# Kernel tuning notes

Hardware: AMD Instinct MI355X
Metric: run time of the kernel (lower is better)

Reference implementation:

```python
import jax, jax.numpy as jnp
import numpy as np

D_MODEL = 1024
N_HEADS = 16
RANK = 128
N_COMPRESS = 16
N_KNOWLEDGE = 32768
KNOWLEDGE_K = 8
B, S = 4, 1024
EPS = 1e-5


def setup_inputs() -> dict:
    key = jax.random.key(0)
    ks = jax.random.split(key, 16)
    inp = {
        'x': jax.random.normal(ks[0], (B, S, D_MODEL), jnp.float32),
        'mask': jnp.tril(jnp.ones((S, S), bool))[None, None],  # causal [1,1,S,S]
        'compress_neurons': jax.random.normal(ks[1], (N_COMPRESS, D_MODEL, RANK), jnp.float32) / np.sqrt(D_MODEL),
        'knowledge_K': jax.random.normal(ks[2], (N_KNOWLEDGE, RANK), jnp.float32) * 0.02,
        'knowledge_V': jax.random.normal(ks[3], (N_KNOWLEDGE, D_MODEL), jnp.float32) * 0.02,
        'router_Q': jax.random.normal(ks[4], (D_MODEL, N_COMPRESS), jnp.float32) * 0.02,
        'router_K': jax.random.normal(ks[5], (D_MODEL, N_COMPRESS), jnp.float32) * 0.02,
        'router_V': jax.random.normal(ks[6], (D_MODEL, N_COMPRESS), jnp.float32) * 0.02,
        'router_M': jax.random.normal(ks[7], (D_MODEL, N_COMPRESS), jnp.float32) * 0.02,
        'W_Q': jax.random.normal(ks[8], (RANK, D_MODEL), jnp.float32) / np.sqrt(RANK),
        'W_K': jax.random.normal(ks[9], (RANK, D_MODEL), jnp.float32) / np.sqrt(RANK),
        'W_V': jax.random.normal(ks[10], (RANK, D_MODEL), jnp.float32) / np.sqrt(RANK),
        'W_O': jax.random.normal(ks[11], (D_MODEL, D_MODEL), jnp.float32) / np.sqrt(D_MODEL),
        'ln1_g': jnp.ones((D_MODEL,), jnp.float32),
        'ln1_b': jnp.zeros((D_MODEL,), jnp.float32),
        'ln2_g': jnp.ones((D_MODEL,), jnp.float32),
        'ln2_b': jnp.zeros((D_MODEL,), jnp.float32),
    }
    return inp


def _layernorm(x, g, b):
    mu = x.mean(-1, keepdims=True)
    var = ((x - mu) ** 2).mean(-1, keepdims=True)
    return (x - mu) * jax.lax.rsqrt(var + EPS) * g + b


def _compress(x, router_W, neurons):
    # x: [B,S,D]; router_W: [D,N]; neurons: [N,D,R]
    weights = jax.nn.softmax(x @ router_W, axis=-1)               # [B,S,N]
    all_proj = jnp.einsum('bsd,ndr->bsnr', x, neurons)            # [B,S,N,R]
    return jnp.einsum('bsnr,bsn->bsr', all_proj, weights)         # [B,S,R]


def reference(x, mask, compress_neurons, knowledge_K, knowledge_V,
              router_Q, router_K, router_V, router_M,
              W_Q, W_K, W_V, W_O, ln1_g, ln1_b, ln2_g, ln2_b):
    d_head = D_MODEL // N_HEADS
    h = _layernorm(x, ln1_g, ln1_b)
    # soft-routed low-rank compression for Q/K/V
    hQ = _compress(h, router_Q, compress_neurons)
    hK = _compress(h, router_K, compress_neurons)
    hV = _compress(h, router_V, compress_neurons)
    Q = (hQ @ W_Q).reshape(B, S, N_HEADS, d_head).transpose(0, 2, 1, 3)
    K = (hK @ W_K).reshape(B, S, N_HEADS, d_head).transpose(0, 2, 1, 3)
    V = (hV @ W_V).reshape(B, S, N_HEADS, d_head).transpose(0, 2, 1, 3)
    scores = jnp.einsum('bhqd,bhkd->bhqk', Q, K) / np.sqrt(d_head)
    scores = jnp.where(mask, scores, -jnp.inf)
    attn = jax.nn.softmax(scores, axis=-1)
    attn_out = jnp.einsum('bhqk,bhkd->bhqd', attn, V)
    attn_out = attn_out.transpose(0, 2, 1, 3).reshape(B, S, D_MODEL)
    x = x + attn_out @ W_O
    # knowledge memory
    h2 = _layernorm(x, ln2_g, ln2_b)
    Qm = _compress(h2, router_M, compress_neurons)                # [B,S,R]
    kscores = Qm @ knowledge_K.T / np.sqrt(RANK)                  # [B,S,NK]
    topk_scores, topk_idx = jax.lax.top_k(kscores, KNOWLEDGE_K)
    kweights = jax.nn.softmax(topk_scores, axis=-1)               # [B,S,k]
    selected_V = knowledge_V[topk_idx]                            # [B,S,k,D]
    mem_out = jnp.einsum('bskd,bsk->bsd', selected_V, kweights)
    return x + mem_out
```

## Files before the change

### kernel.cpp

```cpp
#include <hip/hip_runtime.h>
#include <math.h>

#define DM     1024
#define RANK   128
#define NCMP   16
#define NKNOW  32768
#define TOPK   8
#define NROWS  4096
#define NEG_BIG -3.0e38f
#define TK_SPLIT 32
#define TK_KEYS (NKNOW / TK_SPLIT)

typedef __attribute__((ext_vector_type(8))) short s8v;
typedef __attribute__((ext_vector_type(4))) float f4v;

__device__ __forceinline__ unsigned short f2bf(float f) {
  union { float fl; unsigned u; } v; v.fl = f;
  return (unsigned short)((v.u + 0x7FFFu + ((v.u >> 16) & 1u)) >> 16);
}
__device__ __forceinline__ float bf2f(unsigned short u) {
  return __uint_as_float((unsigned)u << 16);
}
__device__ __forceinline__ f4v mfma16(s8v a, s8v b, f4v c) {
  return __builtin_amdgcn_mfma_f32_16x16x32_bf16(a, b, c, 0, 0, 0);
}
__device__ __forceinline__ unsigned umed3(unsigned a, unsigned b, unsigned c) {
  unsigned d;
  asm("v_med3_u32 %0, %1, %2, %3" : "=v"(d) : "v"(a), "v"(b), "v"(c));
  return d;
}
__device__ __forceinline__ void gload16(const unsigned short* g, unsigned short* l) {
  __builtin_amdgcn_global_load_lds(
      (const __attribute__((address_space(1))) unsigned int*)(g),
      (__attribute__((address_space(3))) unsigned int*)(l), 16, 0, 0);
}

__global__ __launch_bounds__(256) void ln_kernel(const float* __restrict__ x,
                                                 const float* __restrict__ g,
                                                 const float* __restrict__ b,
                                                 unsigned short* __restrict__ obf) {
  __shared__ float red1[4], red2[4];
  const int row = blockIdx.x, t = threadIdx.x;
  const float4 v = reinterpret_cast<const float4*>(x + (size_t)row * DM)[t];
  float s = v.x + v.y + v.z + v.w;
#pragma unroll
  for (int m = 1; m <= 32; m <<= 1) s += __shfl_xor(s, m);
  if ((t & 63) == 0) red1[t >> 6] = s;
  __syncthreads();
  const float mu = (red1[0] + red1[1] + red1[2] + red1[3]) * (1.0f / DM);
  const float dx = v.x - mu, dy = v.y - mu, dz = v.z - mu, dw = v.w - mu;
  float ss = dx * dx + dy * dy + dz * dz + dw * dw;
#pragma unroll
  for (int m = 1; m <= 32; m <<= 1) ss += __shfl_xor(ss, m);
  if ((t & 63) == 0) red2[t >> 6] = ss;
  __syncthreads();
  const float var = (red2[0] + red2[1] + red2[2] + red2[3]) * (1.0f / DM);
  const float inv = rsqrtf(var + 1e-5f);
  const float4 g4 = reinterpret_cast<const float4*>(g)[t];
  const float4 b4 = reinterpret_cast<const float4*>(b)[t];
  ushort4 u = make_ushort4(f2bf(dx * inv * g4.x + b4.x), f2bf(dy * inv * g4.y + b4.y),
                           f2bf(dz * inv * g4.z + b4.z), f2bf(dw * inv * g4.w + b4.w));
  reinterpret_cast<ushort4*>(obf + (size_t)row * DM)[t] = u;
}

__global__ __launch_bounds__(256) void tcvt_kernel(const float* __restrict__ in,
                                                   unsigned short* __restrict__ out,
                                                   int K, int N) {
  __shared__ float ld[32][33];
  const int bb = blockIdx.z;
  const int k0 = blockIdx.y * 32, n0 = blockIdx.x * 32;
  const int t = threadIdx.x;
  const float* ib = in + (size_t)bb * K * N;
  unsigned short* ob = out + (size_t)bb * K * N;
  const int kl = t >> 3, nl = (t & 7) * 4;
  const float4 v = *reinterpret_cast<const float4*>(&ib[(size_t)(k0 + kl) * N + n0 + nl]);
  ld[kl][nl] = v.x; ld[kl][nl + 1] = v.y; ld[kl][nl + 2] = v.z; ld[kl][nl + 3] = v.w;
  __syncthreads();
  const int nw = t >> 3, kw = (t & 7) * 4;
  ushort4 o = make_ushort4(f2bf(ld[kw][nw]), f2bf(ld[kw + 1][nw]),
                           f2bf(ld[kw + 2][nw]), f2bf(ld[kw + 3][nw]));
  *reinterpret_cast<ushort4*>(&ob[(size_t)(n0 + nw) * K + k0 + kw]) = o;
}

__global__ __launch_bounds__(256) void vtr_kernel(const unsigned short* __restrict__ V,
                                                  unsigned short* __restrict__ Vt) {
  __shared__ unsigned short ld[32][40];
  const int bh = blockIdx.z, b = bh >> 4, hh = bh & 15;
  const int s0 = blockIdx.x * 32, d0 = blockIdx.y * 32;
  const int t = threadIdx.x;
  const int r = t >> 3, c = (t & 7) * 4;
  *reinterpret_cast<ushort4*>(&ld[r][c]) =
      *reinterpret_cast<const ushort4*>(&V[(size_t)(b * 1024 + s0 + r) * DM + hh * 64 + d0 + c]);
  __syncthreads();
  ushort4 o;
  o.x = ld[c + 0][r]; o.y = ld[c + 1][r]; o.z = ld[c + 2][r]; o.w = ld[c + 3][r];
  *reinterpret_cast<ushort4*>(&Vt[((size_t)bh * 64 + d0 + r) * 1024 + s0 + c]) = o;
}

__global__ __launch_bounds__(256) void cvt_kernel(const float* __restrict__ in,
                                                  unsigned short* __restrict__ out, int n8) {
  const int i = blockIdx.x * 256 + threadIdx.x;
  if (i < n8) {
    const float4 a = reinterpret_cast<const float4*>(in)[2 * i];
    const float4 b = reinterpret_cast<const float4*>(in)[2 * i + 1];
    reinterpret_cast<ushort4*>(out)[2 * i] =
        make_ushort4(f2bf(a.x), f2bf(a.y), f2bf(a.z), f2bf(a.w));
    reinterpret_cast<ushort4*>(out)[2 * i + 1] =
        make_ushort4(f2bf(b.x), f2bf(b.y), f2bf(b.z), f2bf(b.w));
  }
}

__global__ __launch_bounds__(256) void router3_kernel(const unsigned short* __restrict__ h,
                                                      const float* __restrict__ R0,
                                                      const float* __restrict__ R1,
                                                      const float* __restrict__ R2,
                                                      float* __restrict__ w0,
                                                      float* __restrict__ w1,
                                                      float* __restrict__ w2) {
  __shared__ float hs[DM];
  __shared__ float red[3][16][17];
  const int row = blockIdx.x, t = threadIdx.x;
  {
    const ushort4 u = reinterpret_cast<const ushort4*>(h + (size_t)row * DM)[t];
    hs[t * 4 + 0] = bf2f(u.x); hs[t * 4 + 1] = bf2f(u.y);
    hs[t * 4 + 2] = bf2f(u.z); hs[t * 4 + 3] = bf2f(u.w);
  }
  __syncthreads();
  const int o = t & 15, seg = t >> 4;
  float a0 = 0.f, a1 = 0.f, a2 = 0.f;
  for (int d = seg * 64; d < seg * 64 + 64; ++d) {
    const float hv = hs[d];
    a0 += hv * R0[d * NCMP + o];
    a1 += hv * R1[d * NCMP + o];
    a2 += hv * R2[d * NCMP + o];
  }
  red[0][seg][o] = a0; red[1][seg][o] = a1; red[2][seg][o] = a2;
  __syncthreads();
  if (t < 48) {
    const int g = t >> 4, oo = t & 15;
    float dot = 0.f;
#pragma unroll
    for (int s = 0; s < 16; ++s) dot += red[g][s][oo];
    float m = dot;
#pragma unroll
    for (int msk = 1; msk < 16; msk <<= 1) m = fmaxf(m, __shfl_xor(m, msk));
    const float e = __expf(dot - m);
    float ssum = e;
#pragma unroll
    for (int msk = 1; msk < 16; msk <<= 1) ssum += __shfl_xor(ssum, msk);
    float* wp = (g == 0) ? w0 : (g == 1) ? w1 : w2;
    wp[(size_t)row * NCMP + oo] = e / ssum;
  }
}

__global__ __launch_bounds__(256) void router_kernel(const unsigned short* __restrict__ h,
                                                     const float* __restrict__ R,
                                                     float* __restrict__ w) {
  __shared__ float hs[DM];
  __shared__ float red[16][17];
  const int row = blockIdx.x, t = threadIdx.x;
  {
    const ushort4 u = reinterpret_cast<const ushort4*>(h + (size_t)row * DM)[t];
    hs[t * 4 + 0] = bf2f(u.x); hs[t * 4 + 1] = bf2f(u.y);
    hs[t * 4 + 2] = bf2f(u.z); hs[t * 4 + 3] = bf2f(u.w);
  }
  __syncthreads();
  const int o = t & 15, seg = t >> 4;
  float acc = 0.f;
  for (int d = seg * 64; d < seg * 64 + 64; ++d) acc += hs[d] * R[d * NCMP + o];
  red[seg][o] = acc;
  __syncthreads();
  if (t < 16) {
    float dot = 0.f;
#pragma unroll
    for (int s = 0; s < 16; ++s) dot += red[s][t];
    float m = dot;
#pragma unroll
    for (int msk = 1; msk < 16; msk <<= 1) m = fmaxf(m, __shfl_xor(m, msk));
    const float e = __expf(dot - m);
    float ssum = e;
#pragma unroll
    for (int msk = 1; msk < 16; msk <<= 1) ssum += __shfl_xor(ssum, msk);
    w[(size_t)row * NCMP + t] = e / ssum;
  }
}

template <bool OUT_BF16, bool RES>
__global__ __launch_bounds__(256) void mfma_nt(const unsigned short* __restrict__ A,
                                               const unsigned short* __restrict__ B,
                                               float* __restrict__ Cf,
                                               unsigned short* __restrict__ Cb,
                                               const float* __restrict__ res,
                                               int M, int N, int K, int bshift) {
  __shared__ unsigned short As[128 * 64];
  __shared__ unsigned short Bs[128 * 64];
  const int t = threadIdx.x;
  const int lane = t & 63, w = t >> 6;
  const int wm = w >> 1, wn = w & 1;
  const int bm = blockIdx.y, bn = blockIdx.x;
  const int l15 = lane & 15, l4 = lane >> 4;
  f4v acc[4][4] = {};
  const int srow = w * 32 + (lane >> 3);
  const int scol = ((lane & 7) ^ (lane >> 3)) * 8;
  const unsigned short* ga = A + (size_t)(bm * 128 + srow) * K + scol;
  const unsigned short* gb = B + (size_t)(bm >> bshift) * ((size_t)N * K) +
                             (size_t)(bn * 128 + srow) * K + scol;
  unsigned short* const lA = &As[w * 2048];
  unsigned short* const lB = &Bs[w * 2048];
  for (int k0 = 0; k0 < K; k0 += 64) {
#pragma unroll
    for (int j = 0; j < 4; ++j) {
      gload16(ga + (size_t)j * 8 * K + k0, lA + j * 512);
      gload16(gb + (size_t)j * 8 * K + k0, lB + j * 512);
    }
    __syncthreads();
#pragma unroll
    for (int ks = 0; ks < 2; ++ks) {
      s8v af[4], bf[4];
      const int sc = (ks * 32 + l4 * 8) ^ ((l15 & 7) * 8);
#pragma unroll
      for (int i = 0; i < 4; ++i) {
        af[i] = *reinterpret_cast<const s8v*>(&As[(wm * 64 + i * 16 + l15) * 64 + sc]);
        bf[i] = *reinterpret_cast<const s8v*>(&Bs[(wn * 64 + i * 16 + l15) * 64 + sc]);
      }
#pragma unroll
      for (int i = 0; i < 4; ++i)
#pragma unroll
        for (int j = 0; j < 4; ++j) acc[i][j] = mfma16(af[i], bf[j], acc[i][j]);
    }
    __syncthreads();
  }
#pragma unroll
  for (int i = 0; i < 4; ++i) {
#pragma unroll
    for (int j = 0; j < 4; ++j) {
#pragma unroll
      for (int r = 0; r < 4; ++r) {
        const int row = bm * 128 + wm * 64 + i * 16 + l4 * 4 + r;
        const int col = bn * 128 + wn * 64 + j * 16 + l15;
        float v = acc[i][j][r];
        if constexpr (RES) v += res[(size_t)row * N + col];
        if constexpr (OUT_BF16) Cb[(size_t)row * N + col] = f2bf(v);
        else Cf[(size_t)row * N + col] = v;
      }
    }
  }
}

__global__ __launch_bounds__(128) void wsum_kernel(const unsigned short* __restrict__ ap,
                                                   const float* __restrict__ w0,
                                                   const float* __restrict__ w1,
                                                   const float* __restrict__ w2,
                                                   unsigned short* __restrict__ o0,
                                                   unsigned short* __restrict__ o1,
                                                   unsigned short* __restrict__ o2,
                                                   float scale) {
  const int row = blockIdx.x, r = threadIdx.x;
  float wa[16], wb[16], wc[16];
#pragma unroll
  for (int n = 0; n < 16; ++n) wa[n] = w0[(size_t)row * NCMP + n];
  if (w1) {
#pragma unroll
    for (int n = 0; n < 16; ++n) wb[n] = w1[(size_t)row * NCMP + n];
  }
  if (w2) {
#pragma unroll
    for (int n = 0; n < 16; ++n) wc[n] = w2[(size_t)row * NCMP + n];
  }
  float a0 = 0.f, a1 = 0.f, a2 = 0.f;
  const unsigned short* apr = ap + (size_t)row * (NCMP * RANK) + r;
#pragma unroll
  for (int n = 0; n < 16; ++n) {
    const float v = bf2f(apr[n * RANK]);
    a0 += v * wa[n];
    if (w1) a1 += v * wb[n];
    if (w2) a2 += v * wc[n];
  }
  o0[(size_t)row * RANK + r] = f2bf(a0 * scale);
  if (o1) o1[(size_t)row * RANK + r] = f2bf(a1 * scale);
  if (o2) o2[(size_t)row * RANK + r] = f2bf(a2 * scale);
}

__global__ __launch_bounds__(256) void flash_kernel(const unsigned short* __restrict__ Q,
                                                    const unsigned short* __restrict__ K,
                                                    const unsigned short* __restrict__ Vt,
                                                    unsigned short* __restrict__ O) {
  __shared__ unsigned short Qs[64 * 72], Ks[64 * 72], Vs[64 * 72], Ps[64 * 72];
  const int bh = blockIdx.x, qt = blockIdx.y;
  const int b = bh >> 4, hh = bh & 15;
  const int base = b * 1024, q0 = qt * 64, col = hh * 64;
  const int t = threadIdx.x;
  const int lane = t & 63, w = t >> 6;
  const int l15 = lane & 15, l4 = lane >> 4;
  const int sr = t >> 2, soff = (t & 3) * 16;
  const unsigned short* Vh = Vt + (size_t)bh * 64 * 1024;
  *reinterpret_cast<s8v*>(&Qs[sr * 72 + soff]) =
      *reinterpret_cast<const s8v*>(&Q[(size_t)(base + q0 + sr) * DM + col + soff]);
  *reinterpret_cast<s8v*>(&Qs[sr * 72 + soff + 8]) =
      *reinterpret_cast<const s8v*>(&Q[(size_t)(base + q0 + sr) * DM + col + soff + 8]);
  *reinterpret_cast<s8v*>(&Ks[sr * 72 + soff]) =
      *reinterpret_cast<const s8v*>(&K[(size_t)(base + sr) * DM + col + soff]);
  *reinterpret_cast<s8v*>(&Ks[sr * 72 + soff + 8]) =
      *reinterpret_cast<const s8v*>(&K[(size_t)(base + sr) * DM + col + soff + 8]);
  *reinterpret_cast<s8v*>(&Vs[sr * 72 + soff]) =
      *reinterpret_cast<const s8v*>(&Vh[(size_t)sr * 1024 + soff]);
  *reinterpret_cast<s8v*>(&Vs[sr * 72 + soff + 8]) =
      *reinterpret_cast<const s8v*>(&Vh[(size_t)sr * 1024 + soff + 8]);
  float m_r[4], l_r[4];
  f4v o[4] = {};
#pragma unroll
  for (int r = 0; r < 4; ++r) { m_r[r] = NEG_BIG; l_r[r] = 0.f; }
  __syncthreads();
  for (int kt = 0; kt <= qt; ++kt) {
    const int k0 = kt * 64;
    const bool pre = kt < qt;
    s8v stk0, stk1, stv0, stv1;
    if (pre) {
      const int kn = k0 + 64;
      stk0 = *reinterpret_cast<const s8v*>(&K[(size_t)(base + kn + sr) * DM + col + soff]);
      stk1 = *reinterpret_cast<const s8v*>(&K[(size_t)(base + kn + sr) * DM + col + soff + 8]);
      stv0 = *reinterpret_cast<const s8v*>(&Vh[(size_t)sr * 1024 + kn + soff]);
      stv1 = *reinterpret_cast<const s8v*>(&Vh[(size_t)sr * 1024 + kn + soff + 8]);
    }
    f4v s[4] = {};
#pragma unroll
    for (int ks = 0; ks < 2; ++ks) {
      s8v a = *reinterpret_cast<const s8v*>(&Qs[(w * 16 + l15) * 72 + ks * 32 + l4 * 8]);
#pragma unroll
      for (int nj = 0; nj < 4; ++nj) {
        s8v bb = *reinterpret_cast<const s8v*>(&Ks[(nj * 16 + l15) * 72 + ks * 32 + l4 * 8]);
        s[nj] = mfma16(a, bb, s[nj]);
      }
    }
#pragma unroll
    for (int r = 0; r < 4; ++r) {
      const int grow = q0 + w * 16 + l4 * 4 + r;
      float sv[4];
#pragma unroll
      for (int nj = 0; nj < 4; ++nj) {
        const float xx = s[nj][r] * 0.125f;
        const int gcol = k0 + nj * 16 + l15;
        sv[nj] = (gcol <= grow) ? xx : NEG_BIG;
      }
      float mt = fmaxf(fmaxf(sv[0], sv[1]), fmaxf(sv[2], sv[3]));
#pragma unroll
      for (int msk = 1; msk < 16; msk <<= 1) mt = fmaxf(mt, __shfl_xor(mt, msk));
      const float mn = fmaxf(m_r[r], mt);
      const float sc = __expf(m_r[r] - mn);
      m_r[r] = mn;
      float rs = 0.f, pv[4];
#pragma unroll
      for (int nj = 0; nj < 4; ++nj) { pv[nj] = __expf(sv[nj] - mn); rs += pv[nj]; }
#pragma unroll
      for (int msk = 1; msk < 16; msk <<= 1) rs += __shfl_xor(rs, msk);
      l_r[r] = l_r[r] * sc + rs;
#pragma unroll
      for (int nd = 0; nd < 4; ++nd) o[nd][r] *= sc;
#pragma unroll
      for (int nj = 0; nj < 4; ++nj)
        Ps[(w * 16 + l4 * 4 + r) * 72 + nj * 16 + l15] = f2bf(pv[nj]);
    }
#pragma unroll
    for (int ks = 0; ks < 2; ++ks) {
      s8v pa = *reinterpret_cast<const s8v*>(&Ps[(w * 16 + l15) * 72 + ks * 32 + l4 * 8]);
#pragma unroll
      for (int nd = 0; nd < 4; ++nd) {
        s8v vb = *reinterpret_cast<const s8v*>(&Vs[(nd * 16 + l15) * 72 + ks * 32 + l4 * 8]);
        o[nd] = mfma16(pa, vb, o[nd]);
      }
    }
    __syncthreads();
    if (pre) {
      *reinterpret_cast<s8v*>(&Ks[sr * 72 + soff]) = stk0;
      *reinterpret_cast<s8v*>(&Ks[sr * 72 + soff + 8]) = stk1;
      *reinterpret_cast<s8v*>(&Vs[sr * 72 + soff]) = stv0;
      *reinterpret_cast<s8v*>(&Vs[sr * 72 + soff + 8]) = stv1;
    }
    __syncthreads();
  }
#pragma unroll
  for (int nd = 0; nd < 4; ++nd)
#pragma unroll
    for (int r = 0; r < 4; ++r) {
      const int grow = base + q0 + w * 16 + l4 * 4 + r;
      O[(size_t)grow * DM + col + nd * 16 + l15] = f2bf(o[nd][r] / l_r[r]);
    }
}

__global__ __launch_bounds__(256) void topk_kernel(const unsigned short* __restrict__ Qm,
                                                   const unsigned short* __restrict__ kK,
                                                   float* __restrict__ tks,
                                                   int* __restrict__ tki) {
  __shared__ __align__(16) char arena[32768];
  unsigned short* const Kt0 = (unsigned short*)arena;
  unsigned short* const Kt1 = (unsigned short*)(arena + 16384);
  const int rb = blockIdx.x, sp = blockIdx.y;
  const int r0 = rb * 64, kb0 = sp * TK_KEYS;
  const int t = threadIdx.x;
  const int lane = t & 63, w = t >> 6;
  const int l15 = lane & 15, l4 = lane >> 4;
  s8v qf[4];
#pragma unroll
  for (int ks = 0; ks < 4; ++ks)
    qf[ks] = *reinterpret_cast<const s8v*>(
        &Qm[(size_t)(r0 + w * 16 + l15) * RANK + ks * 32 + l4 * 8]);
  unsigned bs0 = 0u, bs1 = 0u, bs2 = 0u, bs3 = 0u, bs4 = 0u, bs5 = 0u, bs6 = 0u, bs7 = 0u;
  const unsigned short* gkl = kK + (size_t)(kb0 + w * 16 + l15) * RANK + l4 * 8;
  unsigned short* const lw0 = Kt0 + w * 2048;
  unsigned short* const lw1 = Kt1 + w * 2048;
  const int NCH = TK_KEYS / 64;
#pragma unroll
  for (int j = 0; j < 4; ++j) gload16(gkl + j * 32, lw0 + j * 512);
  __syncthreads();
  for (int ch = 0; ch < NCH; ++ch) {
    const unsigned short* const bufc = (ch & 1) ? Kt1 : Kt0;
    unsigned short* const lwn = (ch & 1) ? lw0 : lw1;
    if (ch + 1 < NCH) {
      const unsigned short* g = gkl + (size_t)(ch + 1) * 64 * RANK;
#pragma unroll
      for (int j = 0; j < 4; ++j) gload16(g + j * 32, lwn + j * 512);
    }
    f4v acc[4] = {};
#pragma unroll
    for (int kt = 0; kt < 4; ++kt) {
#pragma unroll
      for (int ks = 0; ks < 4; ++ks) {
        s8v a = *reinterpret_cast<const s8v*>(&bufc[(kt * 4 + ks) * 512 + lane * 8]);
        acc[kt] = mfma16(a, qf[ks], acc[kt]);
      }
    }
    const unsigned invbase = 2047u - (unsigned)(ch * 64 + l4 * 4);
#pragma unroll
    for (int kt = 0; kt < 4; ++kt) {
#pragma unroll
      for (int r = 0; r < 4; ++r) {
        const unsigned u = __float_as_uint(acc[kt][r]);
        const unsigned ord = u ^ ((unsigned)((int)u >> 31) | 0x80000000u);
        const unsigned pk = (ord & 0xFFFFF800u) | (invbase - (unsigned)(kt * 16 + r));
        bs7 = umed3(bs6, pk, bs7);
        bs6 = umed3(bs5, pk, bs6);
        bs5 = umed3(bs4, pk, bs5);
        bs4 = umed3(bs3, pk, bs4);
        bs3 = umed3(bs2, pk, bs3);
        bs2 = umed3(bs1, pk, bs2);
        bs1 = umed3(bs0, pk, bs1);
        bs0 = max(bs0, pk);
      }
    }
    __syncthreads();
  }
  unsigned* const M = (unsigned*)arena;
  const int row = w * 16 + l15;
  {
    unsigned* mp = M + row * 33 + l4 * 8;
    mp[0] = bs0; mp[1] = bs1; mp[2] = bs2; mp[3] = bs3;
    mp[4] = bs4; mp[5] = bs5; mp[6] = bs6; mp[7] = bs7;
  }
  __syncthreads();
  if (t < 64) {
    const unsigned* mr = M + t * 33;
    int h0 = 0, h1 = 0, h2 = 0, h3 = 0;
    const size_t oo = ((size_t)sp * NROWS + r0 + t) * TOPK;
    for (int k = 0; k < TOPK; ++k) {
      const unsigned c0 = (h0 < 8) ? mr[0 + h0] : 0u;
      const unsigned c1 = (h1 < 8) ? mr[8 + h1] : 0u;
      const unsigned c2 = (h2 < 8) ? mr[16 + h2] : 0u;
      const unsigned c3 = (h3 < 8) ? mr[24 + h3] : 0u;
      const unsigned m01 = (c0 >= c1) ? c0 : c1; const int l01 = (c0 >= c1) ? 0 : 1;
      const unsigned m23 = (c2 >= c3) ? c2 : c3; const int l23 = (c2 >= c3) ? 2 : 3;
      const unsigned bst = (m01 >= m23) ? m01 : m23;
      const int bl = (m01 >= m23) ? l01 : l23;
      const unsigned hi = bst & 0xFFFFF800u;
      const unsigned vb = (hi & 0x80000000u) ? (hi & 0x7FFFFFFFu) : ~hi;
      tks[oo + k] = __uint_as_float(vb);
      tki[oo + k] = kb0 + (int)((~bst) & 0x7FFu);
      h0 += (bl == 0); h1 += (bl == 1); h2 += (bl == 2); h3 += (bl == 3);
    }
  }
}

__global__ __launch_bounds__(256) void gather_kernel(const float* __restrict__ tks,
                                                     const int* __restrict__ tki,
                                                     const float* __restrict__ kV,
                                                     float* __restrict__ out) {
  __shared__ float ls[TK_SPLIT * TOPK];
  __shared__ int li[TK_SPLIT * TOPK];
  __shared__ float selv[TOPK];
  __shared__ int seli[TOPK];
  __shared__ float wsel[TOPK];
  const int row = blockIdx.x, t = threadIdx.x;
  if (t < TK_SPLIT * TOPK) {
    const int l = t >> 3, k = t & 7;
    ls[t] = tks[((size_t)l * NROWS + row) * TOPK + k];
    li[t] = tki[((size_t)l * NROWS + row) * TOPK + k];
  }
  __syncthreads();
  if (t < TK_SPLIT * TOPK) {
    const float v = ls[t];
    const int myid = li[t];
    int rank = 0;
    for (int j = 0; j < TK_SPLIT * TOPK; ++j) {
      const float u = ls[j];
      rank += (u > v) || (u == v && li[j] < myid);
    }
    if (rank < TOPK) { selv[rank] = v; seli[rank] = myid; }
  }
  __syncthreads();
  if (t == 0) {
    const float m = selv[0];
    float sum = 0.f, e[TOPK];
#pragma unroll
    for (int k = 0; k < TOPK; ++k) { e[k] = __expf(selv[k] - m); sum += e[k]; }
    const float inv = 1.f / sum;
#pragma unroll
    for (int k = 0; k < TOPK; ++k) wsel[k] = e[k] * inv;
  }
  __syncthreads();
  float4 accv = reinterpret_cast<float4*>(out + (size_t)row * DM)[t];
#pragma unroll
  for (int k = 0; k < TOPK; ++k) {
    const float4 v4 = reinterpret_cast<const float4*>(kV + (size_t)seli[k] * DM)[t];
    const float wk = wsel[k];
    accv.x += wk * v4.x; accv.y += wk * v4.y; accv.z += wk * v4.z; accv.w += wk * v4.w;
  }
  reinterpret_cast<float4*>(out + (size_t)row * DM)[t] = accv;
}

extern "C" void kernel_launch(void* const* d_in, const int* in_sizes, int n_in,
                              void* d_out, int out_size, void* d_ws, size_t ws_size,
                              hipStream_t stream) {
  (void)in_sizes; (void)n_in; (void)out_size; (void)ws_size;
  const float* x    = (const float*)d_in[0];
  const float* neur = (const float*)d_in[2];
  const float* kK   = (const float*)d_in[3];
  const float* kV   = (const float*)d_in[4];
  const float* rQ   = (const float*)d_in[5];
  const float* rK   = (const float*)d_in[6];
  const float* rV   = (const float*)d_in[7];
  const float* rM   = (const float*)d_in[8];
  const float* WQ   = (const float*)d_in[9];
  const float* WK   = (const float*)d_in[10];
  const float* WV   = (const float*)d_in[11];
  const float* WO   = (const float*)d_in[12];
  const float* g1   = (const float*)d_in[13];
  const float* b1   = (const float*)d_in[14];
  const float* g2   = (const float*)d_in[15];
  const float* b2   = (const float*)d_in[16];
  float* out = (float*)d_out;

  char* base = (char*)d_ws;
  auto alloc = [&](size_t bytes) { char* r = base; base += (bytes + 255) & ~(size_t)255; return r; };
  unsigned short* hbf   = (unsigned short*)alloc((size_t)NROWS * DM * 2);
  unsigned short* apb   = (unsigned short*)alloc((size_t)3 * NROWS * DM * 2);
  unsigned short* neurT = (unsigned short*)alloc((size_t)NCMP * RANK * DM * 2);
  unsigned short* WQKVt = (unsigned short*)alloc((size_t)3 * DM * RANK * 2);
  unsigned short* WOt   = (unsigned short*)alloc((size_t)DM * DM * 2);
  unsigned short* kKb   = (unsigned short*)alloc((size_t)NKNOW * RANK * 2);
  unsigned short* hQKVb = (unsigned short*)alloc((size_t)3 * NROWS * RANK * 2);
  unsigned short* Qmb   = (unsigned short*)alloc((size_t)NROWS * RANK * 2);
  unsigned short* Vtb   = (unsigned short*)alloc((size_t)NROWS * DM * 2);
  float* wQw = (float*)alloc((size_t)NROWS * NCMP * 4);
  float* wKw = (float*)alloc((size_t)NROWS * NCMP * 4);
  float* wVw = (float*)alloc((size_t)NROWS * NCMP * 4);
  float* wMw = (float*)alloc((size_t)NROWS * NCMP * 4);
  float* tks = (float*)alloc((size_t)TK_SPLIT * NROWS * TOPK * 4);
  int*   tki = (int*)alloc((size_t)TK_SPLIT * NROWS * TOPK * 4);
  unsigned short* Qb = apb;
  unsigned short* Kb = Qb + (size_t)NROWS * DM;
  unsigned short* Vb = Kb + (size_t)NROWS * DM;
  unsigned short* attnb = hbf;
  unsigned short* hQb = hQKVb;
  unsigned short* hKb = hQKVb + (size_t)NROWS * RANK;
  unsigned short* hVb = hQKVb + (size_t)2 * NROWS * RANK;

  cvt_kernel<<<(NKNOW * RANK / 8 + 255) / 256, 256, 0, stream>>>(kK, kKb, NKNOW * RANK / 8);
  tcvt_kernel<<<dim3(RANK / 32, DM / 32, NCMP), 256, 0, stream>>>(neur, neurT, DM, RANK);
  tcvt_kernel<<<dim3(DM / 32, RANK / 32, 1), 256, 0, stream>>>(WQ, WQKVt, RANK, DM);
  tcvt_kernel<<<dim3(DM / 32, RANK / 32, 1), 256, 0, stream>>>(WK, WQKVt + (size_t)DM * RANK, RANK, DM);
  tcvt_kernel<<<dim3(DM / 32, RANK / 32, 1), 256, 0, stream>>>(WV, WQKVt + (size_t)2 * DM * RANK, RANK, DM);
  tcvt_kernel<<<dim3(DM / 32, DM / 32, 1), 256, 0, stream>>>(WO, WOt, DM, DM);

  ln_kernel<<<NROWS, 256, 0, stream>>>(x, g1, b1, hbf);
  mfma_nt<true, false><<<dim3(16, 32), 256, 0, stream>>>(hbf, neurT, nullptr, apb, nullptr,
                                                         NROWS, NCMP * RANK, DM, 30);
  router3_kernel<<<NROWS, 256, 0, stream>>>(hbf, rQ, rK, rV, wQw, wKw, wVw);
  wsum_kernel<<<NROWS, 128, 0, stream>>>(apb, wQw, wKw, wVw, hQb, hKb, hVb, 1.0f);
  mfma_nt<true, false><<<dim3(8, 96), 256, 0, stream>>>(hQKVb, WQKVt, nullptr, Qb, nullptr,
                                                        3 * NROWS, DM, RANK, 5);
  vtr_kernel<<<dim3(32, 2, 64), 256, 0, stream>>>(Vb, Vtb);
  flash_kernel<<<dim3(64, 16), 256, 0, stream>>>(Qb, Kb, Vtb, attnb);
  mfma_nt<false, true><<<dim3(8, 32), 256, 0, stream>>>(attnb, WOt, out, nullptr, x,
                                                        NROWS, DM, DM, 30);

  ln_kernel<<<NROWS, 256, 0, stream>>>(out, g2, b2, hbf);
  mfma_nt<true, false><<<dim3(16, 32), 256, 0, stream>>>(hbf, neurT, nullptr, apb, nullptr,
                                                         NROWS, NCMP * RANK, DM, 30);
  router_kernel<<<NROWS, 256, 0, stream>>>(hbf, rM, wMw);
  wsum_kernel<<<NROWS, 128, 0, stream>>>(apb, wMw, nullptr, nullptr, Qmb, nullptr, nullptr,
                                         0.08838834764831845f );
  topk_kernel<<<dim3(64, TK_SPLIT), 256, 0, stream>>>(Qmb, kKb, tks, tki);
  gather_kernel<<<NROWS, 256, 0, stream>>>(tks, tki, kV, out);
}
```

Measured before the change: 342.7 us.

## Merge weight-prep launches into one kernel and shrink topk LDS chunk

The kK conversion and the five weight transpose-convert launches are folded into one prep kernel that dispatches on block index. This removes several launch gaps and small-grid tail effects. Separately, the top-k scoring kernel now streams 32 keys per chunk instead of 64, which halves its shared-memory arena to allow more resident blocks per CU. The cost is twice as many chunk iterations and barriers, and the post-loop merge now has to fit in the smaller arena.

```diff
diff --git a/kernel.cpp b/kernel.cpp
--- a/kernel.cpp
+++ b/kernel.cpp
@@ -63,15 +63,13 @@
   reinterpret_cast<ushort4*>(obf + (size_t)row * DM)[t] = u;
 }
 
-__global__ __launch_bounds__(256) void tcvt_kernel(const float* __restrict__ in,
-                                                   unsigned short* __restrict__ out,
-                                                   int K, int N) {
+__device__ __forceinline__ void tcvt_body(const float* __restrict__ in,
+                                          unsigned short* __restrict__ out,
+                                          int K, int N, int bx, int by, int bz, int t) {
   __shared__ float ld[32][33];
-  const int bb = blockIdx.z;
-  const int k0 = blockIdx.y * 32, n0 = blockIdx.x * 32;
-  const int t = threadIdx.x;
-  const float* ib = in + (size_t)bb * K * N;
-  unsigned short* ob = out + (size_t)bb * K * N;
+  const int k0 = by * 32, n0 = bx * 32;
+  const float* ib = in + (size_t)bz * K * N;
+  unsigned short* ob = out + (size_t)bz * K * N;
   const int kl = t >> 3, nl = (t & 7) * 4;
   const float4 v = *reinterpret_cast<const float4*>(&ib[(size_t)(k0 + kl) * N + n0 + nl]);
   ld[kl][nl] = v.x; ld[kl][nl + 1] = v.y; ld[kl][nl + 2] = v.z; ld[kl][nl + 3] = v.w;
@@ -80,6 +78,43 @@
   ushort4 o = make_ushort4(f2bf(ld[kw][nw]), f2bf(ld[kw + 1][nw]),
                            f2bf(ld[kw + 2][nw]), f2bf(ld[kw + 3][nw]));
   *reinterpret_cast<ushort4*>(&ob[(size_t)(n0 + nw) * K + k0 + kw]) = o;
+}
+
+__global__ __launch_bounds__(256) void prep_kernel(const float* __restrict__ kK,
+                                                   unsigned short* __restrict__ kKb,
+                                                   const float* __restrict__ neur,
+                                                   unsigned short* __restrict__ neurT,
+                                                   const float* __restrict__ WQ,
+                                                   const float* __restrict__ WK,
+                                                   const float* __restrict__ WV,
+                                                   unsigned short* __restrict__ WQKVt,
+                                                   const float* __restrict__ WO,
+                                                   unsigned short* __restrict__ WOt) {
+  const int bid = blockIdx.x, t = threadIdx.x;
+  if (bid < 2048) {
+    const int i = bid * 256 + t;
+    const float4 a = reinterpret_cast<const float4*>(kK)[2 * i];
+    const float4 b = reinterpret_cast<const float4*>(kK)[2 * i + 1];
+    reinterpret_cast<ushort4*>(kKb)[2 * i] =
+        make_ushort4(f2bf(a.x), f2bf(a.y), f2bf(a.z), f2bf(a.w));
+    reinterpret_cast<ushort4*>(kKb)[2 * i + 1] =
+        make_ushort4(f2bf(b.x), f2bf(b.y), f2bf(b.z), f2bf(b.w));
+  } else if (bid < 4096) {
+    const int lb = bid - 2048;
+    tcvt_body(neur, neurT, DM, RANK, lb & 3, (lb >> 2) & 31, lb >> 7, t);
+  } else if (bid < 4224) {
+    const int lb = bid - 4096;
+    tcvt_body(WQ, WQKVt, RANK, DM, lb & 31, lb >> 5, 0, t);
+  } else if (bid < 4352) {
+    const int lb = bid - 4224;
+    tcvt_body(WK, WQKVt + (size_t)DM * RANK, RANK, DM, lb & 31, lb >> 5, 0, t);
+  } else if (bid < 4480) {
+    const int lb = bid - 4352;
+    tcvt_body(WV, WQKVt + (size_t)2 * DM * RANK, RANK, DM, lb & 31, lb >> 5, 0, t);
+  } else {
+    const int lb = bid - 4480;
+    tcvt_body(WO, WOt, DM, DM, lb & 31, lb >> 5, 0, t);
+  }
 }
 
 __global__ __launch_bounds__(256) void vtr_kernel(const unsigned short* __restrict__ V,
@@ -95,19 +130,6 @@
   ushort4 o;
   o.x = ld[c + 0][r]; o.y = ld[c + 1][r]; o.z = ld[c + 2][r]; o.w = ld[c + 3][r];
   *reinterpret_cast<ushort4*>(&Vt[((size_t)bh * 64 + d0 + r) * 1024 + s0 + c]) = o;
-}
-
-__global__ __launch_bounds__(256) void cvt_kernel(const float* __restrict__ in,
-                                                  unsigned short* __restrict__ out, int n8) {
-  const int i = blockIdx.x * 256 + threadIdx.x;
-  if (i < n8) {
-    const float4 a = reinterpret_cast<const float4*>(in)[2 * i];
-    const float4 b = reinterpret_cast<const float4*>(in)[2 * i + 1];
-    reinterpret_cast<ushort4*>(out)[2 * i] =
-        make_ushort4(f2bf(a.x), f2bf(a.y), f2bf(a.z), f2bf(a.w));
-    reinterpret_cast<ushort4*>(out)[2 * i + 1] =
-        make_ushort4(f2bf(b.x), f2bf(b.y), f2bf(b.z), f2bf(b.w));
-  }
 }
 
 __global__ __launch_bounds__(256) void router3_kernel(const unsigned short* __restrict__ h,
@@ -391,9 +413,9 @@
                                                    const unsigned short* __restrict__ kK,
                                                    float* __restrict__ tks,
                                                    int* __restrict__ tki) {
-  __shared__ __align__(16) char arena[32768];
+  __shared__ __align__(16) char arena[16384];
   unsigned short* const Kt0 = (unsigned short*)arena;
-  unsigned short* const Kt1 = (unsigned short*)(arena + 16384);
+  unsigned short* const Kt1 = (unsigned short*)(arena + 8192);
   const int rb = blockIdx.x, sp = blockIdx.y;
   const int r0 = rb * 64, kb0 = sp * TK_KEYS;
   const int t = threadIdx.x;
@@ -405,33 +427,33 @@
     qf[ks] = *reinterpret_cast<const s8v*>(
         &Qm[(size_t)(r0 + w * 16 + l15) * RANK + ks * 32 + l4 * 8]);
   unsigned bs0 = 0u, bs1 = 0u, bs2 = 0u, bs3 = 0u, bs4 = 0u, bs5 = 0u, bs6 = 0u, bs7 = 0u;
-  const unsigned short* gkl = kK + (size_t)(kb0 + w * 16 + l15) * RANK + l4 * 8;
-  unsigned short* const lw0 = Kt0 + w * 2048;
-  unsigned short* const lw1 = Kt1 + w * 2048;
-  const int NCH = TK_KEYS / 64;
-#pragma unroll
-  for (int j = 0; j < 4; ++j) gload16(gkl + j * 32, lw0 + j * 512);
+  const int s0i = 2 * w, s1i = 2 * w + 1;
+  const unsigned short* g0 = kK + (size_t)(kb0 + (s0i >> 2) * 16 + l15) * RANK + (s0i & 3) * 32 + l4 * 8;
+  const unsigned short* g1 = kK + (size_t)(kb0 + (s1i >> 2) * 16 + l15) * RANK + (s1i & 3) * 32 + l4 * 8;
+  const int NCH = TK_KEYS / 32;
+  gload16(g0, Kt0 + s0i * 512);
+  gload16(g1, Kt0 + s1i * 512);
   __syncthreads();
   for (int ch = 0; ch < NCH; ++ch) {
     const unsigned short* const bufc = (ch & 1) ? Kt1 : Kt0;
-    unsigned short* const lwn = (ch & 1) ? lw0 : lw1;
+    unsigned short* const bufn = (ch & 1) ? Kt0 : Kt1;
     if (ch + 1 < NCH) {
-      const unsigned short* g = gkl + (size_t)(ch + 1) * 64 * RANK;
-#pragma unroll
-      for (int j = 0; j < 4; ++j) gload16(g + j * 32, lwn + j * 512);
-    }
-    f4v acc[4] = {};
-#pragma unroll
-    for (int kt = 0; kt < 4; ++kt) {
+      const size_t off = (size_t)(ch + 1) * 32 * RANK;
+      gload16(g0 + off, bufn + s0i * 512);
+      gload16(g1 + off, bufn + s1i * 512);
+    }
+    f4v acc[2] = {};
+#pragma unroll
+    for (int kt = 0; kt < 2; ++kt) {
 #pragma unroll
       for (int ks = 0; ks < 4; ++ks) {
         s8v a = *reinterpret_cast<const s8v*>(&bufc[(kt * 4 + ks) * 512 + lane * 8]);
         acc[kt] = mfma16(a, qf[ks], acc[kt]);
       }
     }
-    const unsigned invbase = 2047u - (unsigned)(ch * 64 + l4 * 4);
-#pragma unroll
-    for (int kt = 0; kt < 4; ++kt) {
+    const unsigned invbase = 2047u - (unsigned)(ch * 32 + l4 * 4);
+#pragma unroll
+    for (int kt = 0; kt < 2; ++kt) {
 #pragma unroll
       for (int r = 0; r < 4; ++r) {
         const unsigned u = __float_as_uint(acc[kt][r]);
@@ -573,12 +595,7 @@
   unsigned short* hKb = hQKVb + (size_t)NROWS * RANK;
   unsigned short* hVb = hQKVb + (size_t)2 * NROWS * RANK;
 
-  cvt_kernel<<<(NKNOW * RANK / 8 + 255) / 256, 256, 0, stream>>>(kK, kKb, NKNOW * RANK / 8);
-  tcvt_kernel<<<dim3(RANK / 32, DM / 32, NCMP), 256, 0, stream>>>(neur, neurT, DM, RANK);
-  tcvt_kernel<<<dim3(DM / 32, RANK / 32, 1), 256, 0, stream>>>(WQ, WQKVt, RANK, DM);
-  tcvt_kernel<<<dim3(DM / 32, RANK / 32, 1), 256, 0, stream>>>(WK, WQKVt + (size_t)DM * RANK, RANK, DM);
-  tcvt_kernel<<<dim3(DM / 32, RANK / 32, 1), 256, 0, stream>>>(WV, WQKVt + (size_t)2 * DM * RANK, RANK, DM);
-  tcvt_kernel<<<dim3(DM / 32, DM / 32, 1), 256, 0, stream>>>(WO, WOt, DM, DM);
+  prep_kernel<<<5504, 256, 0, stream>>>(kK, kKb, neur, neurT, WQ, WK, WV, WQKVt, WO, WOt);
 
   ln_kernel<<<NROWS, 256, 0, stream>>>(x, g1, b1, hbf);
   mfma_nt<true, false><<<dim3(16, 32), 256, 0, stream>>>(hbf, neurT, nullptr, apb, nullptr,
```

Measured after the change: 336.5 us. About the same (-1.8%).
